# Kernel optimization log

Hardware: AMD Instinct MI355X
Metric: run time of the kernel (lower is better)

## Reference

```python
import jax, jax.numpy as jnp
import numpy as np
from jax import lax

EPS_BN = 1e-5
EPS_ADD = 1e-12


def _bn2d(x, g, b):
    # train-mode BatchNorm2d: stats over (N,H,W), biased variance
    m = x.mean(axis=(0, 2, 3), keepdims=True)
    v = x.var(axis=(0, 2, 3), keepdims=True)
    return (x - m) * lax.rsqrt(v + EPS_BN) * g[None, :, None, None] + b[None, :, None, None]


def _bn1d(x, g, b):
    # train-mode BatchNorm1d on [B,C,L]: stats over (N,L)
    m = x.mean(axis=(0, 2), keepdims=True)
    v = x.var(axis=(0, 2), keepdims=True)
    return (x - m) * lax.rsqrt(v + EPS_BN) * g[None, :, None] + b[None, :, None]


def _addw(w, a, b):
    wr = jax.nn.relu(w)
    wn = wr / (wr.sum() + EPS_ADD)
    return wn[0] * a + wn[1] * b


def setup_inputs() -> dict:
    key = jax.random.key(0)
    B, C, L = 16, 128, 16384
    H = 8
    ks = jax.random.split(key, 16)
    inp = {
        "x": jax.random.normal(ks[0], (B, C, L), dtype=jnp.float32),
        "dw_w": jax.random.normal(ks[1], (3, C, 1, 3, 3), dtype=jnp.float32) * 0.1,
        "bn2_g": jnp.ones((3, C), jnp.float32),
        "bn2_b": jnp.zeros((3, C), jnp.float32),
        "pw_w": jax.random.normal(ks[2], (3, C, C), dtype=jnp.float32) * 0.05,
        "pw_b": jax.random.normal(ks[3], (3, C), dtype=jnp.float32) * 0.02,
        "add_w": jnp.ones((2,), jnp.float32),
        "bn1_g": jnp.ones((C,), jnp.float32),
        "bn1_b": jnp.zeros((C,), jnp.float32),
        "W1": jax.random.normal(ks[4], (C, C // 4), dtype=jnp.float32) * 0.05,
        "b1": jnp.zeros((C // 4,), jnp.float32),
        "W2": jax.random.normal(ks[5], (C // 4, C), dtype=jnp.float32) * 0.05,
        "b2": jnp.zeros((C,), jnp.float32),
        "ffn_add_w": jnp.ones((2,), jnp.float32),
        "ffn_bn_g": jnp.ones((C,), jnp.float32),
        "ffn_bn_b": jnp.zeros((C,), jnp.float32),
        "heads": 8,
    }
    return inp


def reference(x, dw_w, bn2_g, bn2_b, pw_w, pw_b, add_w, bn1_g, bn1_b,
              W1, b1, W2, b2, ffn_add_w, ffn_bn_g, ffn_bn_b, heads):
    B, C, L = x.shape
    S = int(np.sqrt(L))  # static perfect-square side
    maps = x.reshape(B, C, S, S)

    # q (stride 1), k, v (stride 2) branches: depthwise3x3 -> BN2d -> pointwise1x1 -> GELU
    outs = []
    for i, st in enumerate((1, 2, 2)):
        y = lax.conv_general_dilated(
            maps, dw_w[i], window_strides=(st, st), padding=[(1, 1), (1, 1)],
            feature_group_count=C, dimension_numbers=("NCHW", "OIHW", "NCHW"))
        y = _bn2d(y, bn2_g[i], bn2_b[i])
        y = jnp.einsum("oc,bchw->bohw", pw_w[i], y) + pw_b[i][None, :, None, None]
        outs.append(jax.nn.gelu(y, approximate=False))
    q, k, v = outs

    def flat(t):  # [B,C,h,w] -> [B, n, C]
        return t.reshape(t.shape[0], t.shape[1], -1).transpose(0, 2, 1)

    q, k, v = flat(q), flat(k), flat(v)  # q: [B,L,C]; k,v: [B,L/4,C]
    dh = C // heads
    qh = q.reshape(B, -1, heads, dh)
    kh = k.reshape(B, -1, heads, dh)
    vh = v.reshape(B, -1, heads, dh)
    qs = jax.nn.softmax(qh, axis=-1)      # softmax over per-head channel dim
    ks_ = jax.nn.softmax(kh, axis=1)      # softmax over key sequence dim
    kv = jnp.einsum("bnhd,bnhe->bhde", ks_, vh)   # [B,H,dh,dh] tiny
    att = jnp.einsum("blhd,bhde->blhe", qs, kv)   # [B,L,H,dh]
    mhlsa = att.transpose(0, 2, 3, 1).reshape(B, C, L)  # concat heads on channel

    att_out = _bn1d(_addw(add_w, mhlsa, x), bn1_g, bn1_b)  # [B,C,L]

    # FFN on [B,L,C]
    f = jax.nn.gelu(jnp.einsum("blc,cf->blf", att_out.transpose(0, 2, 1), W1) + b1, approximate=False)
    f = jax.nn.gelu(jnp.einsum("blf,fc->blc", f, W2) + b2, approximate=False)
    out = _bn1d(_addw(ffn_add_w, f.transpose(0, 2, 1), att_out), ffn_bn_g, ffn_bn_b)
    return out
```

## Files before the change

kernel.cpp:

```cpp
#include <hip/hip_runtime.h>
#include <hip/hip_bf16.h>
#include <math.h>

#define BB 16
#define CC 128
#define LL 16384
#define SS 128
#define LK 4096
#define NHEAD 8
#define DH 16

typedef __attribute__((ext_vector_type(8))) short short8;
typedef __attribute__((ext_vector_type(4))) float f32x4;

__device__ __forceinline__ float gelu_f(float x) {
    return 0.5f * x * (1.0f + erff(x * 0.70710678118654752f));
}

__device__ __forceinline__ ushort f2bf(float f) {
    __hip_bfloat16 h = __float2bfloat16(f);
    return *(ushort*)&h;
}
__device__ __forceinline__ float bf2f(ushort u) {
    union { unsigned int i; float f; } x; x.i = ((unsigned int)u) << 16; return x.f;
}

__device__ __forceinline__ void block_reduce2(float& s1, float& s2) {
    #pragma unroll
    for (int off = 32; off; off >>= 1) {
        s1 += __shfl_down(s1, off);
        s2 += __shfl_down(s2, off);
    }
    __shared__ float red[2][4];
    int wid = threadIdx.x >> 6, lid = threadIdx.x & 63;
    if (lid == 0) { red[0][wid] = s1; red[1][wid] = s2; }
    __syncthreads();
    if (threadIdx.x == 0) {
        int nw = blockDim.x >> 6;
        float a = 0.f, b = 0.f;
        for (int i = 0; i < nw; i++) { a += red[0][i]; b += red[1][i]; }
        s1 = a; s2 = b;
    }
}

__global__ __launch_bounds__(256) void k_dw(const float* __restrict__ x,
        const float* __restrict__ dw_w,
        ushort* __restrict__ dwq, ushort* __restrict__ dwk, ushort* __restrict__ dwv) {
    int bx = blockIdx.x;
    int cg = bx & 3;
    int oh = (bx >> 2) & 127;
    int b  = bx >> 9;
    __shared__ float xs[3][32][132];
    __shared__ float wls[3][32][9];
    int tid = threadIdx.x;
    for (int i = tid; i < 864; i += 256) {
        int br = i / 288; int rem = i - br * 288; int c = rem / 9; int tap = rem - c * 9;
        wls[br][c][tap] = dw_w[(br * CC + cg * 32 + c) * 9 + tap];
    }
    for (int i = tid; i < 3 * 32 * 32; i += 256) {
        int r = i >> 10;
        int rem = i & 1023;
        int c = rem >> 5;
        int f4 = rem & 31;
        int ih = oh - 1 + r;
        float4 v = make_float4(0.f, 0.f, 0.f, 0.f);
        if (ih >= 0 && ih < 128)
            v = *(const float4*)(x + ((size_t)b * CC + cg * 32 + c) * (size_t)LL + ih * SS + f4 * 4);
        *(float4*)&xs[r][c][f4 * 4] = v;
    }
    __syncthreads();
    int owb = tid & 63;
    int q4 = tid >> 6;
    union { ushort u[8]; float4 v; } pk;
    #pragma unroll
    for (int pass = 0; pass < 2; pass++) {
        int ow = owb + pass * 64;
        #pragma unroll
        for (int cc = 0; cc < 8; cc++) {
            int c = q4 * 8 + cc;
            float acc = 0.f;
            #pragma unroll
            for (int r = 0; r < 3; r++) {
                #pragma unroll
                for (int d = 0; d < 3; d++) {
                    int iw = ow + d - 1;
                    if (iw >= 0 && iw < 128) acc += wls[0][c][r * 3 + d] * xs[r][c][iw];
                }
            }
            pk.u[cc] = f2bf(acc);
        }
        *(float4*)(dwq + ((((size_t)b * 4 + cg) * LL) + oh * 128 + ow) * 32 + q4 * 8) = pk.v;
    }
    if ((oh & 1) == 0) {
        int ohp = oh >> 1;
        int owp = owb;
        #pragma unroll
        for (int br = 1; br <= 2; br++) {
            #pragma unroll
            for (int cc = 0; cc < 8; cc++) {
                int c = q4 * 8 + cc;
                float acc = 0.f;
                #pragma unroll
                for (int r = 0; r < 3; r++) {
                    #pragma unroll
                    for (int d = 0; d < 3; d++) {
                        int iw = 2 * owp + d - 1;
                        if (iw >= 0) acc += wls[br][c][r * 3 + d] * xs[r][c][iw];
                    }
                }
                pk.u[cc] = f2bf(acc);
            }
            ushort* dst = (br == 1) ? dwk : dwv;
            *(float4*)(dst + ((((size_t)b * 4 + cg) * LK) + ohp * 64 + owp) * 32 + q4 * 8) = pk.v;
        }
    }
}

__global__ __launch_bounds__(256) void k_stats_dw(const ushort* __restrict__ dwq,
        const ushort* __restrict__ dwk, const ushort* __restrict__ dwv,
        float* __restrict__ stats ) {
    int bx = blockIdx.x;
    int br, b, cg, rows;
    const ushort* base;
    if (bx < 256) {
        br = 0; b = bx >> 4; cg = (bx >> 2) & 3; int chunk = bx & 3;
        base = dwq + (((size_t)b * 4 + cg) * LL + chunk * 4096) * 32; rows = 4096;
    } else {
        int i = bx - 256; br = 1 + (i >> 6); int j = i & 63; b = j >> 2; cg = j & 3;
        base = ((br == 1) ? dwk : dwv) + (((size_t)b * 4 + cg) * LK) * 32; rows = 4096;
    }
    int tid = threadIdx.x;
    int quad = tid & 3;
    float s1[8], s2[8];
    #pragma unroll
    for (int i = 0; i < 8; i++) { s1[i] = 0.f; s2[i] = 0.f; }
    for (int r = tid >> 2; r < rows; r += 64) {
        union { ushort u[8]; float4 v; } pk;
        pk.v = *(const float4*)(base + (size_t)r * 32 + quad * 8);
        #pragma unroll
        for (int i = 0; i < 8; i++) { float f = bf2f(pk.u[i]); s1[i] += f; s2[i] += f * f; }
    }
    __shared__ float a1[32], a2[32];
    if (tid < 32) { a1[tid] = 0.f; a2[tid] = 0.f; }
    __syncthreads();
    #pragma unroll
    for (int i = 0; i < 8; i++) {
        atomicAdd(&a1[quad * 8 + i], s1[i]);
        atomicAdd(&a2[quad * 8 + i], s2[i]);
    }
    __syncthreads();
    if (tid < 32) {
        atomicAdd(&stats[(br * CC + cg * 32 + tid) * 2 + 0], a1[tid]);
        atomicAdd(&stats[(br * CC + cg * 32 + tid) * 2 + 1], a2[tid]);
    }
}

__global__ void k_finalize_dw(const float* __restrict__ stats, const float* __restrict__ pw_w,
                              const float* __restrict__ pw_b, const float* __restrict__ bn2_g,
                              const float* __restrict__ bn2_b,
                              ushort* __restrict__ effWb, float* __restrict__ effB) {
    int br = blockIdx.x >> 7;
    int o  = blockIdx.x & 127;
    int c  = threadIdx.x;
    float N = (br == 0) ? 262144.f : 65536.f;
    float s1 = stats[(br * CC + c) * 2 + 0];
    float s2 = stats[(br * CC + c) * 2 + 1];
    float m = s1 / N;
    float v = s2 / N - m * m;
    float sc = rsqrtf(v + 1e-5f);
    float A  = bn2_g[br * CC + c] * sc;
    float Bc = bn2_b[br * CC + c] - m * A;
    float w  = pw_w[((size_t)br * CC + o) * CC + c];
    effWb[((size_t)br * CC + o) * CC + c] = f2bf(w * A);
    float pb = w * Bc, dummy = 0.f;
    block_reduce2(pb, dummy);
    if (threadIdx.x == 0) effB[br * CC + o] = pw_b[br * CC + o] + pb;
}

__global__ __launch_bounds__(256) void k_gemm_kv(const ushort* __restrict__ dwk,
        const ushort* __restrict__ dwv, const ushort* __restrict__ effWb,
        const float* __restrict__ effB, float* __restrict__ kbuf, float* __restrict__ vbuf) {
    __shared__ __align__(16) char raw[69632];
    short* As = (short*)raw;
    short* Bs = (short*)(raw + 34816);
    float* Sf = (float*)raw;
    int bx = blockIdx.x;
    int brv = bx >> 9;
    int b = (bx >> 5) & 15;
    int p0 = (bx & 31) * 128;
    const ushort* dw = brv ? dwv : dwk;
    const ushort* Wg = effWb + (size_t)(1 + brv) * CC * CC;
    int tid = threadIdx.x;
    for (int i = tid; i < 2048; i += 256) {
        int row = i >> 4; int f4 = i & 15; int cg = f4 >> 2;
        float4 v = *(const float4*)(dw + (((size_t)b * 4 + cg) * LK + p0 + row) * 32 + (f4 & 3) * 8);
        *(float4*)&As[row * 136 + f4 * 8] = v;
    }
    for (int i = tid; i < 2048; i += 256) {
        int row = i >> 4; int f4 = i & 15;
        float4 v = *(const float4*)(Wg + (size_t)row * 128 + f4 * 8);
        *(float4*)&Bs[row * 136 + f4 * 8] = v;
    }
    __syncthreads();
    int w = tid >> 6, l = tid & 63;
    int m0 = w * 32;
    int la = l & 15, lb = l >> 4;
    f32x4 acc[2][8];
    #pragma unroll
    for (int i = 0; i < 2; i++)
        #pragma unroll
        for (int j = 0; j < 8; j++) acc[i][j] = (f32x4){0.f, 0.f, 0.f, 0.f};
    #pragma unroll
    for (int kt = 0; kt < 4; kt++) {
        int kb = kt * 32 + lb * 8;
        short8 a0 = *(const short8*)&As[(m0 + la) * 136 + kb];
        short8 a1 = *(const short8*)&As[(m0 + 16 + la) * 136 + kb];
        #pragma unroll
        for (int nt = 0; nt < 8; nt++) {
            short8 bf = *(const short8*)&Bs[(nt * 16 + la) * 136 + kb];
            acc[0][nt] = __builtin_amdgcn_mfma_f32_16x16x32_bf16(a0, bf, acc[0][nt], 0, 0, 0);
            acc[1][nt] = __builtin_amdgcn_mfma_f32_16x16x32_bf16(a1, bf, acc[1][nt], 0, 0, 0);
        }
    }
    __syncthreads();
    float bias[8];
    #pragma unroll
    for (int nt = 0; nt < 8; nt++) bias[nt] = effB[(1 + brv) * CC + nt * 16 + la];
    #pragma unroll
    for (int mt = 0; mt < 2; mt++)
        #pragma unroll
        for (int nt = 0; nt < 8; nt++)
            #pragma unroll
            for (int i = 0; i < 4; i++) {
                float vv = acc[mt][nt][i] + bias[nt];
                Sf[(m0 + mt * 16 + lb * 4 + i) * 132 + nt * 16 + la] = gelu_f(vv);
            }
    __syncthreads();
    float* outb = (brv ? vbuf : kbuf) + ((size_t)b * LK + p0) * CC;
    for (int i = tid; i < 4096; i += 256) {
        int row = i >> 5; int c4 = i & 31;
        *(float4*)(outb + (size_t)row * CC + c4 * 4) = *(const float4*)&Sf[row * 132 + c4 * 4];
    }
}

__global__ void k_kv_accum(const float* __restrict__ k_buf, const float* __restrict__ v_buf,
                           float* __restrict__ kv_un, float* __restrict__ ssum) {
    int bx = blockIdx.x;
    int b = bx >> 5;
    int h = (bx >> 2) & 7;
    int sl = bx & 3;
    int n0 = sl * 1024;
    __shared__ float kch[64][16];
    __shared__ float vch[64][16];
    int tid = threadIdx.x;
    int d = tid >> 4, e = tid & 15;
    float acc = 0.f, ss = 0.f;
    for (int ch = 0; ch < 16; ch++) {
        int base = n0 + ch * 64;
        {
            int rr = tid >> 2, c4 = (tid & 3) * 4;
            const float* kp = k_buf + ((size_t)b * LK + base + rr) * CC + h * DH + c4;
            const float* vp = v_buf + ((size_t)b * LK + base + rr) * CC + h * DH + c4;
            float4 kf = *(const float4*)kp;
            float4 vf = *(const float4*)vp;
            kch[rr][c4+0] = __expf(kf.x); kch[rr][c4+1] = __expf(kf.y);
            kch[rr][c4+2] = __expf(kf.z); kch[rr][c4+3] = __expf(kf.w);
            vch[rr][c4+0] = vf.x; vch[rr][c4+1] = vf.y;
            vch[rr][c4+2] = vf.z; vch[rr][c4+3] = vf.w;
        }
        __syncthreads();
        #pragma unroll 8
        for (int rr = 0; rr < 64; rr++) {
            float ek = kch[rr][d];
            acc += ek * vch[rr][e];
            ss += ek;
        }
        __syncthreads();
    }
    atomicAdd(&kv_un[(((size_t)b * NHEAD + h) * DH + d) * DH + e], acc);
    if (e == 0) atomicAdd(&ssum[((size_t)b * NHEAD + h) * DH + d], ss);
}

__global__ void k_kv_div(const float* __restrict__ kv_un, const float* __restrict__ ssum,
                         float* __restrict__ kv) {
    int i = blockIdx.x * 256 + threadIdx.x;
    kv[i] = kv_un[i] / ssum[i >> 4];
}

__global__ __launch_bounds__(256) void k_gemm_q(const ushort* __restrict__ dwq,
        const ushort* __restrict__ effWb, const float* __restrict__ effB,
        const float* __restrict__ kvb, const float* __restrict__ add_w,
        const float* __restrict__ x, float* __restrict__ y1) {
    __shared__ __align__(16) char raw[69632];
    short* As = (short*)raw;
    short* Bs = (short*)(raw + 34816);
    float* Sf = (float*)raw;
    __shared__ float kvs[2048];
    int bx = blockIdx.x;
    int b = bx >> 7;
    int p0 = (bx & 127) * 128;
    int tid = threadIdx.x;
    for (int i = tid; i < 512; i += 256)
        *(float4*)&kvs[i * 4] = *(const float4*)(kvb + (size_t)b * 2048 + i * 4);
    for (int i = tid; i < 2048; i += 256) {
        int row = i >> 4; int f4 = i & 15; int cg = f4 >> 2;
        float4 v = *(const float4*)(dwq + (((size_t)b * 4 + cg) * LL + p0 + row) * 32 + (f4 & 3) * 8);
        *(float4*)&As[row * 136 + f4 * 8] = v;
    }
    for (int i = tid; i < 2048; i += 256) {
        int row = i >> 4; int f4 = i & 15;
        float4 v = *(const float4*)(effWb + (size_t)row * 128 + f4 * 8);
        *(float4*)&Bs[row * 136 + f4 * 8] = v;
    }
    __syncthreads();
    int w = tid >> 6, l = tid & 63;
    int m0 = w * 32;
    int la = l & 15, lb = l >> 4;
    f32x4 acc[2][8];
    #pragma unroll
    for (int i = 0; i < 2; i++)
        #pragma unroll
        for (int j = 0; j < 8; j++) acc[i][j] = (f32x4){0.f, 0.f, 0.f, 0.f};
    #pragma unroll
    for (int kt = 0; kt < 4; kt++) {
        int kb = kt * 32 + lb * 8;
        short8 a0 = *(const short8*)&As[(m0 + la) * 136 + kb];
        short8 a1 = *(const short8*)&As[(m0 + 16 + la) * 136 + kb];
        #pragma unroll
        for (int nt = 0; nt < 8; nt++) {
            short8 bf = *(const short8*)&Bs[(nt * 16 + la) * 136 + kb];
            acc[0][nt] = __builtin_amdgcn_mfma_f32_16x16x32_bf16(a0, bf, acc[0][nt], 0, 0, 0);
            acc[1][nt] = __builtin_amdgcn_mfma_f32_16x16x32_bf16(a1, bf, acc[1][nt], 0, 0, 0);
        }
    }
    __syncthreads();
    float bias[8];
    #pragma unroll
    for (int nt = 0; nt < 8; nt++) bias[nt] = effB[nt * 16 + la];
    #pragma unroll
    for (int mt = 0; mt < 2; mt++)
        #pragma unroll
        for (int nt = 0; nt < 8; nt++)
            #pragma unroll
            for (int i = 0; i < 4; i++) {
                float vv = acc[mt][nt][i] + bias[nt];
                Sf[(m0 + mt * 16 + lb * 4 + i) * 133 + nt * 16 + la] = gelu_f(vv);
            }
    __syncthreads();
    int p = tid & 127;
    int hg = tid >> 7;
    float wa0 = add_w[0], wa1 = add_w[1];
    float r0 = fmaxf(wa0, 0.f), r1 = fmaxf(wa1, 0.f);
    float inv = 1.f / (r0 + r1 + 1e-12f);
    float wn0 = r0 * inv, wn1 = r1 * inv;
    const float* xb = x + (size_t)b * CC * (size_t)LL + p0 + p;
    float* yb = y1 + (size_t)b * CC * (size_t)LL + p0 + p;
    #pragma unroll
    for (int hh = 0; hh < 4; hh++) {
        int h = hg * 4 + hh;
        float sv[16];
        float mx = -1e30f;
        #pragma unroll
        for (int d = 0; d < 16; d++) { sv[d] = Sf[p * 133 + h * 16 + d]; mx = fmaxf(mx, sv[d]); }
        float s = 0.f;
        #pragma unroll
        for (int d = 0; d < 16; d++) { sv[d] = __expf(sv[d] - mx); s += sv[d]; }
        float is = 1.f / s;
        #pragma unroll
        for (int e = 0; e < 16; e++) {
            float att = 0.f;
            #pragma unroll
            for (int d = 0; d < 16; d++) att += sv[d] * kvs[(h * 16 + d) * 16 + e];
            int c = h * 16 + e;
            yb[(size_t)c * LL] = wn0 * att * is + wn1 * xb[(size_t)c * LL];
        }
    }
}

__global__ void k_chan_stats(const float* __restrict__ buf, float* __restrict__ stats) {
    int c = blockIdx.x >> 5;
    int s = blockIdx.x & 31;
    int b = s >> 1;
    int p0 = (s & 1) << 13;
    const float* src = buf + (size_t)b * (CC * (size_t)LL) + (size_t)c * LL + p0;
    float s1 = 0.f, s2 = 0.f;
    for (int i = threadIdx.x * 4; i < 8192; i += 1024) {
        float4 v = *(const float4*)(src + i);
        s1 += v.x + v.y + v.z + v.w;
        s2 += v.x * v.x + v.y * v.y + v.z * v.z + v.w * v.w;
    }
    block_reduce2(s1, s2);
    if (threadIdx.x == 0) {
        atomicAdd(&stats[c * 2 + 0], s1);
        atomicAdd(&stats[c * 2 + 1], s2);
    }
}

__global__ void k_fin1(const float* __restrict__ stats1, const float* __restrict__ bn1_g,
                       const float* __restrict__ bn1_b, const float* __restrict__ W1,
                       const float* __restrict__ b1, const float* __restrict__ W2,
                       float* __restrict__ A1B1, float* __restrict__ effW1,
                       float* __restrict__ effb1, float* __restrict__ W2T) {
    int t = threadIdx.x;
    const float N = 262144.f;
    float m = stats1[t * 2] / N;
    float v = stats1[t * 2 + 1] / N - m * m;
    float sc = rsqrtf(v + 1e-5f);
    float A = bn1_g[t] * sc;
    float Bc = bn1_b[t] - m * A;
    A1B1[t] = A; A1B1[128 + t] = Bc;
    __shared__ float Bs[128];
    Bs[t] = Bc;
    for (int j = 0; j < 32; j++) effW1[t * 32 + j] = W1[t * 32 + j] * A;
    for (int j = 0; j < 32; j++) W2T[t * 32 + j] = W2[j * 128 + t];
    __syncthreads();
    if (t < 32) {
        float s = b1[t];
        for (int c = 0; c < 128; c++) s += W1[c * 32 + t] * Bs[c];
        effb1[t] = s;
    }
}

__global__ __launch_bounds__(256) void k_ffn1(const float* __restrict__ y1,
        const float* __restrict__ effW1, const float* __restrict__ effb1,
        float* __restrict__ f1) {
    __shared__ float wl[4096];
    __shared__ float bl[32];
    int tid = threadIdx.x;
    for (int i = tid; i < 4096; i += 256) wl[i] = effW1[i];
    if (tid < 32) bl[tid] = effb1[tid];
    __syncthreads();
    int gp = blockIdx.x * 256 + tid;
    int b = gp >> 14, p = gp & 16383;
    const float* col = y1 + (size_t)b * (CC * (size_t)LL) + p;
    float acc[32];
    #pragma unroll
    for (int j = 0; j < 32; j++) acc[j] = bl[j];
    for (int c = 0; c < CC; c++) {
        float v = col[(size_t)c * LL];
        const float4* w4 = (const float4*)&wl[c * 32];
        #pragma unroll
        for (int i = 0; i < 8; i++) {
            float4 w = w4[i];
            acc[4*i+0] += w.x * v; acc[4*i+1] += w.y * v;
            acc[4*i+2] += w.z * v; acc[4*i+3] += w.w * v;
        }
    }
    float4* dst = (float4*)(f1 + (size_t)gp * 32);
    #pragma unroll
    for (int i = 0; i < 8; i++) {
        float4 o4;
        o4.x = gelu_f(acc[4*i+0]); o4.y = gelu_f(acc[4*i+1]);
        o4.z = gelu_f(acc[4*i+2]); o4.w = gelu_f(acc[4*i+3]);
        dst[i] = o4;
    }
}

__global__ __launch_bounds__(256) void k_ffn2(const float* __restrict__ f1,
        const float* __restrict__ W2T, const float* __restrict__ b2,
        const float* __restrict__ y1, const float* __restrict__ A1B1,
        const float* __restrict__ ffn_add_w, float* __restrict__ outb) {
    __shared__ float wl[4096];
    __shared__ float b2l[128];
    __shared__ float abl[256];
    int tid = threadIdx.x;
    for (int i = tid; i < 4096; i += 256) wl[i] = W2T[i];
    if (tid < 128) b2l[tid] = b2[tid];
    if (tid >= 128) abl[tid - 128] = A1B1[tid - 128];
    if (tid < 128) abl[128 + tid] = A1B1[128 + tid];
    __syncthreads();
    int gp = blockIdx.x * 256 + tid;
    int b = gp >> 14, p = gp & 16383;
    float f[32];
    {
        const float4* src = (const float4*)(f1 + (size_t)gp * 32);
        #pragma unroll
        for (int i = 0; i < 8; i++) {
            float4 v = src[i];
            f[4*i+0] = v.x; f[4*i+1] = v.y; f[4*i+2] = v.z; f[4*i+3] = v.w;
        }
    }
    float wa0 = ffn_add_w[0], wa1 = ffn_add_w[1];
    float r0 = fmaxf(wa0, 0.f), r1 = fmaxf(wa1, 0.f);
    float inv = 1.f / (r0 + r1 + 1e-12f);
    float wn0 = r0 * inv, wn1 = r1 * inv;
    const float* ycol = y1 + (size_t)b * (CC * (size_t)LL) + p;
    float* ocol = outb + (size_t)b * (CC * (size_t)LL) + p;
    for (int c = 0; c < CC; c++) {
        const float4* w4 = (const float4*)&wl[c * 32];
        float a = b2l[c];
        #pragma unroll
        for (int i = 0; i < 8; i++) {
            float4 w = w4[i];
            a += w.x * f[4*i+0] + w.y * f[4*i+1] + w.z * f[4*i+2] + w.w * f[4*i+3];
        }
        float f2 = gelu_f(a);
        float attv = ycol[(size_t)c * LL] * abl[c] + abl[128 + c];
        ocol[(size_t)c * LL] = wn0 * f2 + wn1 * attv;
    }
}

__global__ void k_fin2(const float* __restrict__ stats2, const float* __restrict__ g,
                       const float* __restrict__ bb, float* __restrict__ A2B2) {
    int t = threadIdx.x;
    const float N = 262144.f;
    float m = stats2[t * 2] / N;
    float v = stats2[t * 2 + 1] / N - m * m;
    float sc = rsqrtf(v + 1e-5f);
    float A = g[t] * sc;
    A2B2[t] = A;
    A2B2[128 + t] = bb[t] - m * A;
}

__global__ void k_norm(float* __restrict__ out, const float* __restrict__ A2B2) {
    size_t i = ((size_t)blockIdx.x * 256 + threadIdx.x) * 4;
    int c = (int)((i >> 14) & 127);
    float A = A2B2[c], Bc = A2B2[128 + c];
    float4 v = *(float4*)(out + i);
    v.x = v.x * A + Bc; v.y = v.y * A + Bc; v.z = v.z * A + Bc; v.w = v.w * A + Bc;
    *(float4*)(out + i) = v;
}

extern "C" void kernel_launch(void* const* d_in, const int* in_sizes, int n_in,
                              void* d_out, int out_size, void* d_ws, size_t ws_size,
                              hipStream_t stream) {
    const float* x        = (const float*)d_in[0];
    const float* dw_w     = (const float*)d_in[1];
    const float* bn2_g    = (const float*)d_in[2];
    const float* bn2_b    = (const float*)d_in[3];
    const float* pw_w     = (const float*)d_in[4];
    const float* pw_b     = (const float*)d_in[5];
    const float* add_w    = (const float*)d_in[6];
    const float* bn1_g    = (const float*)d_in[7];
    const float* bn1_b    = (const float*)d_in[8];
    const float* W1       = (const float*)d_in[9];
    const float* b1       = (const float*)d_in[10];
    const float* W2       = (const float*)d_in[11];
    const float* b2       = (const float*)d_in[12];
    const float* ffn_aw   = (const float*)d_in[13];
    const float* ffn_bn_g = (const float*)d_in[14];
    const float* ffn_bn_b = (const float*)d_in[15];

    float* w = (float*)d_ws;
    size_t off = 0;
    auto alloc = [&](size_t n) { float* p = w + off; off += n; return p; };
    float* dwstats = alloc(768);
    float* stats1  = alloc(256);
    float* stats2  = alloc(256);
    float* kv_un   = alloc(32768);
    float* ssum    = alloc(2048);
    size_t zero_bytes = off * sizeof(float);
    float* effWb_f = alloc(24576);
    float* effB    = alloc(384);
    float* kvb     = alloc(32768);
    float* A1B1    = alloc(256);
    float* effW1   = alloc(4096);
    float* effb1   = alloc(32);
    float* W2T     = alloc(4096);
    float* A2B2    = alloc(256);
    float* y1      = alloc((size_t)BB * CC * LL);
    float* kbuf    = alloc((size_t)BB * LK * CC);
    float* vbuf    = alloc((size_t)BB * LK * CC);
    float* dwq_f   = alloc((size_t)BB * LL * CC / 2);
    float* dwk_f   = alloc((size_t)BB * LK * CC / 2);
    float* dwv_f   = alloc((size_t)BB * LK * CC / 2);
    float* f1      = kbuf;
    (void)ws_size;

    ushort* effWb = (ushort*)effWb_f;
    ushort* dwq = (ushort*)dwq_f;
    ushort* dwk = (ushort*)dwk_f;
    ushort* dwv = (ushort*)dwv_f;
    float* outf = (float*)d_out;

    hipMemsetAsync(d_ws, 0, zero_bytes, stream);

    k_dw<<<8192, 256, 0, stream>>>(x, dw_w, dwq, dwk, dwv);
    k_stats_dw<<<384, 256, 0, stream>>>(dwq, dwk, dwv, dwstats);
    k_finalize_dw<<<384, 128, 0, stream>>>(dwstats, pw_w, pw_b, bn2_g, bn2_b, effWb, effB);
    k_gemm_kv<<<1024, 256, 0, stream>>>(dwk, dwv, effWb, effB, kbuf, vbuf);
    k_kv_accum<<<512, 256, 0, stream>>>(kbuf, vbuf, kv_un, ssum);
    k_kv_div<<<128, 256, 0, stream>>>(kv_un, ssum, kvb);
    k_gemm_q<<<2048, 256, 0, stream>>>(dwq, effWb, effB, kvb, add_w, x, y1);
    k_chan_stats<<<4096, 256, 0, stream>>>(y1, stats1);
    k_fin1<<<1, 128, 0, stream>>>(stats1, bn1_g, bn1_b, W1, b1, W2, A1B1, effW1, effb1, W2T);
    k_ffn1<<<1024, 256, 0, stream>>>(y1, effW1, effb1, f1);
    k_ffn2<<<1024, 256, 0, stream>>>(f1, W2T, b2, y1, A1B1, ffn_aw, outf);
    k_chan_stats<<<4096, 256, 0, stream>>>(outf, stats2);
    k_fin2<<<1, 128, 0, stream>>>(stats2, ffn_bn_g, ffn_bn_b, A2B2);
    k_norm<<<32768, 256, 0, stream>>>(outf, A2B2);
}
```

Before: 942.5 us.

## Fuse depthwise BN statistics into depthwise conv and register-tile per-channel rows

```diff
diff --git a/kernel.cpp b/kernel.cpp
--- a/kernel.cpp
+++ b/kernel.cpp
@@ -45,113 +45,129 @@
 
 __global__ __launch_bounds__(256) void k_dw(const float* __restrict__ x,
         const float* __restrict__ dw_w,
-        ushort* __restrict__ dwq, ushort* __restrict__ dwk, ushort* __restrict__ dwv) {
+        ushort* __restrict__ dwq, ushort* __restrict__ dwk, ushort* __restrict__ dwv,
+        float* __restrict__ dwstats) {
     int bx = blockIdx.x;
     int cg = bx & 3;
     int oh = (bx >> 2) & 127;
     int b  = bx >> 9;
     __shared__ float xs[3][32][132];
-    __shared__ float wls[3][32][9];
     int tid = threadIdx.x;
-    for (int i = tid; i < 864; i += 256) {
-        int br = i / 288; int rem = i - br * 288; int c = rem / 9; int tap = rem - c * 9;
-        wls[br][c][tap] = dw_w[(br * CC + cg * 32 + c) * 9 + tap];
-    }
+    int cl  = tid >> 3;
+    int owg = tid & 7;
+    int ow0 = owg * 16;
+    int c   = cg * 32 + cl;
+    bool do_kv = ((oh & 1) == 0);
+
+    float wq[9], wk[9], wv[9];
+    const float* wp = dw_w + (size_t)c * 9;
+    #pragma unroll
+    for (int t = 0; t < 9; t++) wq[t] = wp[t];
+    #pragma unroll
+    for (int t = 0; t < 9; t++) wk[t] = wp[(size_t)CC * 9 + t];
+    #pragma unroll
+    for (int t = 0; t < 9; t++) wv[t] = wp[(size_t)2 * CC * 9 + t];
+
     for (int i = tid; i < 3 * 32 * 32; i += 256) {
         int r = i >> 10;
         int rem = i & 1023;
-        int c = rem >> 5;
+        int ch = rem >> 5;
         int f4 = rem & 31;
         int ih = oh - 1 + r;
         float4 v = make_float4(0.f, 0.f, 0.f, 0.f);
         if (ih >= 0 && ih < 128)
-            v = *(const float4*)(x + ((size_t)b * CC + cg * 32 + c) * (size_t)LL + ih * SS + f4 * 4);
-        *(float4*)&xs[r][c][f4 * 4] = v;
-    }
-    __syncthreads();
-    int owb = tid & 63;
-    int q4 = tid >> 6;
-    union { ushort u[8]; float4 v; } pk;
-    #pragma unroll
-    for (int pass = 0; pass < 2; pass++) {
-        int ow = owb + pass * 64;
-        #pragma unroll
-        for (int cc = 0; cc < 8; cc++) {
-            int c = q4 * 8 + cc;
-            float acc = 0.f;
+            v = *(const float4*)(x + ((size_t)b * CC + cg * 32 + ch) * (size_t)LL + ih * SS + f4 * 4);
+        *(float4*)&xs[r][ch][f4 * 4] = v;
+    }
+    if (tid < 96) {
+        int r = tid >> 5, ch = tid & 31;
+        *(float4*)&xs[r][ch][128] = make_float4(0.f, 0.f, 0.f, 0.f);
+    }
+    __syncthreads();
+
+    float aq[16], ak[8], av[8];
+    #pragma unroll
+    for (int j = 0; j < 16; j++) aq[j] = 0.f;
+    #pragma unroll
+    for (int j = 0; j < 8; j++) { ak[j] = 0.f; av[j] = 0.f; }
+
+    #pragma unroll
+    for (int r = 0; r < 3; r++) {
+        const float* row = &xs[r][cl][0];
+        float g[18];
+        g[0] = owg ? row[ow0 - 1] : 0.f;
+        float4 v0 = *(const float4*)&row[ow0];
+        float4 v1 = *(const float4*)&row[ow0 + 4];
+        float4 v2 = *(const float4*)&row[ow0 + 8];
+        float4 v3 = *(const float4*)&row[ow0 + 12];
+        g[1] = v0.x;  g[2] = v0.y;  g[3] = v0.z;  g[4] = v0.w;
+        g[5] = v1.x;  g[6] = v1.y;  g[7] = v1.z;  g[8] = v1.w;
+        g[9] = v2.x;  g[10] = v2.y; g[11] = v2.z; g[12] = v2.w;
+        g[13] = v3.x; g[14] = v3.y; g[15] = v3.z; g[16] = v3.w;
+        g[17] = row[ow0 + 16];
+        float w0 = wq[3 * r], w1 = wq[3 * r + 1], w2 = wq[3 * r + 2];
+        #pragma unroll
+        for (int j = 0; j < 16; j++)
+            aq[j] += w0 * g[j] + w1 * g[j + 1] + w2 * g[j + 2];
+        if (do_kv) {
+            float k0 = wk[3 * r], k1 = wk[3 * r + 1], k2 = wk[3 * r + 2];
+            float x0 = wv[3 * r], x1 = wv[3 * r + 1], x2 = wv[3 * r + 2];
             #pragma unroll
-            for (int r = 0; r < 3; r++) {
-                #pragma unroll
-                for (int d = 0; d < 3; d++) {
-                    int iw = ow + d - 1;
-                    if (iw >= 0 && iw < 128) acc += wls[0][c][r * 3 + d] * xs[r][c][iw];
-                }
+            for (int j = 0; j < 8; j++) {
+                ak[j] += k0 * g[2 * j] + k1 * g[2 * j + 1] + k2 * g[2 * j + 2];
+                av[j] += x0 * g[2 * j] + x1 * g[2 * j + 1] + x2 * g[2 * j + 2];
             }
-            pk.u[cc] = f2bf(acc);
-        }
-        *(float4*)(dwq + ((((size_t)b * 4 + cg) * LL) + oh * 128 + ow) * 32 + q4 * 8) = pk.v;
-    }
-    if ((oh & 1) == 0) {
+        }
+    }
+
+    {
+        size_t qbase = (((size_t)b * 4 + cg) * LL + (size_t)oh * 128) * 32 + cl;
+        float s1 = 0.f, s2 = 0.f;
+        #pragma unroll
+        for (int j = 0; j < 16; j++) {
+            ushort u = f2bf(aq[j]);
+            float fv = bf2f(u);
+            s1 += fv; s2 += fv * fv;
+            dwq[qbase + (size_t)(ow0 + j) * 32] = u;
+        }
+        #pragma unroll
+        for (int m = 1; m <= 4; m <<= 1) {
+            s1 += __shfl_xor(s1, m);
+            s2 += __shfl_xor(s2, m);
+        }
+        if (owg == 0) {
+            atomicAdd(&dwstats[(size_t)c * 2 + 0], s1);
+            atomicAdd(&dwstats[(size_t)c * 2 + 1], s2);
+        }
+    }
+
+    if (do_kv) {
         int ohp = oh >> 1;
-        int owp = owb;
-        #pragma unroll
-        for (int br = 1; br <= 2; br++) {
-            #pragma unroll
-            for (int cc = 0; cc < 8; cc++) {
-                int c = q4 * 8 + cc;
-                float acc = 0.f;
-                #pragma unroll
-                for (int r = 0; r < 3; r++) {
-                    #pragma unroll
-                    for (int d = 0; d < 3; d++) {
-                        int iw = 2 * owp + d - 1;
-                        if (iw >= 0) acc += wls[br][c][r * 3 + d] * xs[r][c][iw];
-                    }
-                }
-                pk.u[cc] = f2bf(acc);
-            }
-            ushort* dst = (br == 1) ? dwk : dwv;
-            *(float4*)(dst + ((((size_t)b * 4 + cg) * LK) + ohp * 64 + owp) * 32 + q4 * 8) = pk.v;
-        }
-    }
-}
-
-__global__ __launch_bounds__(256) void k_stats_dw(const ushort* __restrict__ dwq,
-        const ushort* __restrict__ dwk, const ushort* __restrict__ dwv,
-        float* __restrict__ stats ) {
-    int bx = blockIdx.x;
-    int br, b, cg, rows;
-    const ushort* base;
-    if (bx < 256) {
-        br = 0; b = bx >> 4; cg = (bx >> 2) & 3; int chunk = bx & 3;
-        base = dwq + (((size_t)b * 4 + cg) * LL + chunk * 4096) * 32; rows = 4096;
-    } else {
-        int i = bx - 256; br = 1 + (i >> 6); int j = i & 63; b = j >> 2; cg = j & 3;
-        base = ((br == 1) ? dwk : dwv) + (((size_t)b * 4 + cg) * LK) * 32; rows = 4096;
-    }
-    int tid = threadIdx.x;
-    int quad = tid & 3;
-    float s1[8], s2[8];
-    #pragma unroll
-    for (int i = 0; i < 8; i++) { s1[i] = 0.f; s2[i] = 0.f; }
-    for (int r = tid >> 2; r < rows; r += 64) {
-        union { ushort u[8]; float4 v; } pk;
-        pk.v = *(const float4*)(base + (size_t)r * 32 + quad * 8);
-        #pragma unroll
-        for (int i = 0; i < 8; i++) { float f = bf2f(pk.u[i]); s1[i] += f; s2[i] += f * f; }
-    }
-    __shared__ float a1[32], a2[32];
-    if (tid < 32) { a1[tid] = 0.f; a2[tid] = 0.f; }
-    __syncthreads();
-    #pragma unroll
-    for (int i = 0; i < 8; i++) {
-        atomicAdd(&a1[quad * 8 + i], s1[i]);
-        atomicAdd(&a2[quad * 8 + i], s2[i]);
-    }
-    __syncthreads();
-    if (tid < 32) {
-        atomicAdd(&stats[(br * CC + cg * 32 + tid) * 2 + 0], a1[tid]);
-        atomicAdd(&stats[(br * CC + cg * 32 + tid) * 2 + 1], a2[tid]);
+        size_t kbase = (((size_t)b * 4 + cg) * LK + (size_t)ohp * 64) * 32 + cl;
+        float t1 = 0.f, t2 = 0.f, u1 = 0.f, u2 = 0.f;
+        #pragma unroll
+        for (int j = 0; j < 8; j++) {
+            int owp = owg * 8 + j;
+            ushort uk = f2bf(ak[j]);
+            float fk = bf2f(uk);
+            t1 += fk; t2 += fk * fk;
+            dwk[kbase + (size_t)owp * 32] = uk;
+            ushort uv = f2bf(av[j]);
+            float fv = bf2f(uv);
+            u1 += fv; u2 += fv * fv;
+            dwv[kbase + (size_t)owp * 32] = uv;
+        }
+        #pragma unroll
+        for (int m = 1; m <= 4; m <<= 1) {
+            t1 += __shfl_xor(t1, m); t2 += __shfl_xor(t2, m);
+            u1 += __shfl_xor(u1, m); u2 += __shfl_xor(u2, m);
+        }
+        if (owg == 0) {
+            atomicAdd(&dwstats[((size_t)CC + c) * 2 + 0], t1);
+            atomicAdd(&dwstats[((size_t)CC + c) * 2 + 1], t2);
+            atomicAdd(&dwstats[((size_t)2 * CC + c) * 2 + 0], u1);
+            atomicAdd(&dwstats[((size_t)2 * CC + c) * 2 + 1], u2);
+        }
     }
 }
 
@@ -575,8 +591,7 @@
 
     hipMemsetAsync(d_ws, 0, zero_bytes, stream);
 
-    k_dw<<<8192, 256, 0, stream>>>(x, dw_w, dwq, dwk, dwv);
-    k_stats_dw<<<384, 256, 0, stream>>>(dwq, dwk, dwv, dwstats);
+    k_dw<<<8192, 256, 0, stream>>>(x, dw_w, dwq, dwk, dwv, dwstats);
     k_finalize_dw<<<384, 128, 0, stream>>>(dwstats, pw_w, pw_b, bn2_g, bn2_b, effWb, effB);
     k_gemm_kv<<<1024, 256, 0, stream>>>(dwk, dwv, effWb, effB, kbuf, vbuf);
     k_kv_accum<<<512, 256, 0, stream>>>(kbuf, vbuf, kv_un, ssum);
```

Result: faster. 856.1 us (-9.2%).
